# Kernel tuning notes

Measured on AMD Instinct MI355X. Metric: run time of the kernel, lower is better.

The kernel has to match this reference:

```python
import jax, jax.numpy as jnp
import numpy as np

B, N, RD = 32, 2000, 32
E, H, A = 128, 256, 8
NUM_ACTIONS = N
ACTION_NORM = float(NUM_ACTIONS)


def _mlp2(x, W1, b1, W2, b2):
    return jnp.maximum(x @ W1 + b1, 0.0) @ W2 + b2


def setup_inputs() -> dict:
    key = jax.random.key(0)
    ks = jax.random.split(key, 8)
    s = lambda fan_in: 1.0 / np.sqrt(fan_in)
    return {
        "state": jax.random.normal(ks[0], (B, N, RD), jnp.float32),
        "distance_matrix": jax.random.uniform(ks[1], (N, N), jnp.float32),
        "W_emb1": jax.random.normal(ks[2], (RD, H), jnp.float32) * s(RD),
        "b_emb1": jnp.zeros((H,), jnp.float32),
        "W_emb2": jax.random.normal(ks[3], (H, E), jnp.float32) * s(H),
        "b_emb2": jnp.zeros((E,), jnp.float32),
        "Wq1": jax.random.normal(ks[4], (E + A, H), jnp.float32) * s(E + A),
        "bq1": jnp.zeros((H,), jnp.float32),
        "Wq2": jax.random.normal(ks[5], (H, 1), jnp.float32) * s(H),
        "bq2": jnp.zeros((1,), jnp.float32),
        "fixed_actions": jax.random.randint(ks[6], (3, B), 0, NUM_ACTIONS, jnp.int32),
        "fixed_agent_ids": jnp.arange(3, dtype=jnp.int32),
    }


def reference(state, distance_matrix, W_emb1, b_emb1, W_emb2, b_emb2,
              Wq1, bq1, Wq2, bq2, fixed_actions, fixed_agent_ids):
    # normalized distance -> similarity, row-stochastic
    dm = distance_matrix / distance_matrix.max()
    sim = jnp.exp(-dm)  # scaling = 1 (use_nn_scaling=False)
    sim = sim / sim.sum(-1, keepdims=True)

    enc = _mlp2(state, W_emb1, b_emb1, W_emb2, b_emb2)      # [B,N,E]
    x = jnp.einsum('nm,bme->bne', sim, enc)                 # graph conv mix

    idx_f = jnp.arange(N, dtype=x.dtype)

    def qnet(actions):
        # actions: [B,A] broadcast over node axis -> concat -> MLP -> [B,N]
        act = jnp.broadcast_to(actions[:, None, :], (B, N, A))
        feat = jnp.concatenate([x, act], axis=-1)           # [B,N,E+A]
        return _mlp2(feat, Wq1, bq1, Wq2, bq2)[..., 0]      # [B,N]

    # init actions: -1 everywhere, fixed agents get given action / norm
    actions = jnp.full((B, A), -1.0, dtype=x.dtype)
    actions = actions.at[:, fixed_agent_ids].set(
        fixed_actions.T.astype(x.dtype) / ACTION_NORM)

    # sequential per-agent soft-argmax loop (second torch loop; the first
    # torch loop's q-values are fully overwritten here, so it is dead code)
    q_cols = []
    for agent_id in range(A):
        q = qnet(actions)                                   # [B,N]
        sam = jnp.clip(jax.nn.softmax(q, axis=-1) @ idx_f, 0.0, float(NUM_ACTIONS))
        actions = actions.at[:, agent_id].set(
            jax.lax.stop_gradient(sam / ACTION_NORM))
        q2 = qnet(actions)
        qv = jnp.take_along_axis(q2, sam.astype(jnp.int32)[:, None], axis=-1)[:, 0]
        q_cols.append(qv)

    q_values = jnp.stack(q_cols, axis=1)                    # [B,A]
    chosen = (actions * ACTION_NORM).astype(jnp.int32)      # [B,A]
    return q_values, chosen
```

## Files before the change

### kernel.cpp

```cpp
#include <hip/hip_runtime.h>
#include <cstddef>

#define NB 32
#define NN 2000
#define NRD 32
#define NE 128
#define NH 256
#define NA 8
#define KP8 2048
#define NGP 128
#define H1S 264
#define XTS 136
#define ACTION_NORM 2000.0f

typedef unsigned short u16;
typedef unsigned char u8;
typedef __bf16 b16x8 __attribute__((ext_vector_type(8)));
typedef float f32x4 __attribute__((ext_vector_type(4)));
typedef long lx2 __attribute__((ext_vector_type(2)));
typedef const __attribute__((address_space(1))) unsigned int* gptr_t;
typedef __attribute__((address_space(3))) unsigned int* lptr_t;

__device__ inline u16 f2bf(float x) {
    unsigned u = __float_as_uint(x);
    u += 0x7FFFu + ((u >> 16) & 1u);
    return (u16)(u >> 16);
}
__device__ inline float bf2f(u16 h) { return __uint_as_float((unsigned)h << 16); }
__device__ inline u8 f2fp8(float x) {
    return (u8)(__builtin_amdgcn_cvt_pk_fp8_f32(x, x, 0, false) & 0xFF);
}
__device__ inline u16 f2fp8x2(float a, float b) {
    return (u16)(__builtin_amdgcn_cvt_pk_fp8_f32(a, b, 0, false) & 0xFFFF);
}
__device__ inline float fp82f(u8 b) {
    return __builtin_amdgcn_cvt_pk_f32_fp8((unsigned)b, false)[0];
}
__device__ inline int kswz(int m) {
    return (m & ~63) + (((m >> 3) & 3) << 4) + (((m >> 5) & 1) << 3) + (m & 7);
}

#define PREP_STATE (64000 * 32)
#define PREP_W1T   (256 * 32)
#define PREP_W2T   (128 * 256)
#define PREP_WQ1T  (256 * 128)
#define PREP_PAD   (4096 * 48)
#define PREP_TOT   (PREP_STATE + PREP_W1T + PREP_W2T + PREP_WQ1T + PREP_PAD)
#define PREP_BLOCKS (PREP_TOT / 256)
#define MAX_BLOCKS 1024
__global__ __launch_bounds__(256) void k_front(
        const float* __restrict__ state, const float* __restrict__ W1,
        const float* __restrict__ W2, const float* __restrict__ Wq1,
        const float* __restrict__ dm, const int* __restrict__ fa,
        const int* __restrict__ fid,
        u16* __restrict__ state_b, u16* __restrict__ W1t,
        u16* __restrict__ W2t, u16* __restrict__ Wq1at,
        u8* __restrict__ encb, float* __restrict__ pmax,
        float* __restrict__ actions) {
    __shared__ float sh[256];
    const int blk = blockIdx.x, t = threadIdx.x;
    if (blk < PREP_BLOCKS) {
        int i = blk * 256 + t;
        if (i < PREP_STATE) { state_b[i] = f2bf(state[i]); return; }
        i -= PREP_STATE;
        if (i < PREP_W1T) { int h = i >> 5, k = i & 31; W1t[i] = f2bf(W1[k * NH + h]); return; }
        i -= PREP_W1T;
        if (i < PREP_W2T) { int e = i >> 8, h = i & 255; W2t[i] = f2bf(W2[h * NE + e]); return; }
        i -= PREP_W2T;
        if (i < PREP_WQ1T) { int hq = i >> 7, e = i & 127; Wq1at[i] = f2bf(Wq1[e * NH + hq]); return; }
        i -= PREP_WQ1T;
        if (i < PREP_PAD) { int eb = i / 48, mm = NN + (i % 48); encb[(size_t)eb * KP8 + kswz(mm)] = 0; }
        return;
    }
    if (blk < PREP_BLOCKS + MAX_BLOCKS) {
        const int bid = blk - PREP_BLOCKS;
        float m = 0.0f;
        for (size_t i = (size_t)bid * 256 + t; i < (size_t)NN * NN; i += (size_t)MAX_BLOCKS * 256)
            m = fmaxf(m, dm[i]);
        sh[t] = m; __syncthreads();
        for (int s = 128; s > 0; s >>= 1) {
            if (t < s) sh[t] = fmaxf(sh[t], sh[t + s]);
            __syncthreads();
        }
        if (t == 0) pmax[bid] = sh[0];
        return;
    }
    const int b = t >> 3, a = t & 7;
    float v = -1.0f;
    for (int j = 0; j < 3; ++j)
        if (fid[j] == a) v = (float)fa[j * NB + b] / ACTION_NORM;
    actions[t] = v;
}

__global__ __launch_bounds__(512) void k_sim_enc(
        const u16* __restrict__ state_b, const u16* __restrict__ W1t,
        const u16* __restrict__ W2t, u8* __restrict__ encb,
        const float* __restrict__ b1, const float* __restrict__ b2,
        const float* __restrict__ dm, const float* __restrict__ pmax,
        u8* __restrict__ simb, float* __restrict__ inv_rs) {
    __shared__ u16 stage[20 * 512];
    __shared__ u16 h1t[64 * H1S];
    const int blk = blockIdx.x, tid = threadIdx.x;

    if (blk >= 1000) {
        float* shf = (float*)stage;
        const int n = blk - 1000, t = tid;
        float m = fmaxf(pmax[t], pmax[t + 512]);
        shf[t] = m; __syncthreads();
        for (int s = 256; s > 0; s >>= 1) {
            if (t < s) shf[t] = fmaxf(shf[t], shf[t + s]);
            __syncthreads();
        }
        const float inv = 1.0f / shf[0];
        __syncthreads();
        float s = 0.0f;
        for (int mm = t * 2; mm < KP8; mm += 1024) {
            float e0 = 0.0f, e1 = 0.0f;
            if (mm < NN)     { e0 = expf(-dm[(size_t)n * NN + mm] * inv);     s += e0; }
            if (mm + 1 < NN) { e1 = expf(-dm[(size_t)n * NN + mm + 1] * inv); s += e1; }
            *(u16*)(simb + (size_t)n * KP8 + kswz(mm)) = f2fp8x2(e0, e1);
        }
        shf[t] = s; __syncthreads();
        for (int st = 256; st > 0; st >>= 1) {
            if (t < st) shf[t] += shf[t + st];
            __syncthreads();
        }
        if (t == 0) inv_rs[n] = 1.0f / shf[0];
        return;
    }

    const int w = tid >> 6, l = tid & 63;
    const int lm = l & 15, lq = l >> 4;
    const int gm = blk * 64;

    {
#pragma unroll
        for (int i = 0; i < 3; ++i) {
            const int idx = w * 3 + i;
            if (idx < 20) {
                const u16* gp;
                if (idx < 4) gp = state_b + (size_t)(gm + idx * 16 + lm) * NRD + lq * 8;
                else         gp = W1t + (size_t)((idx - 4) * 16 + lm) * NRD + lq * 8;
                __builtin_amdgcn_global_load_lds((gptr_t)gp, (lptr_t)(stage + idx * 512), 16, 0, 0);
            }
        }
        __syncthreads();
        b16x8 af[4], bf[2];
#pragma unroll
        for (int i = 0; i < 4; ++i) af[i] = *(const b16x8*)(stage + i * 512 + l * 8);
#pragma unroll
        for (int j = 0; j < 2; ++j) bf[j] = *(const b16x8*)(stage + (4 + w * 2 + j) * 512 + l * 8);
        f32x4 acc1[4][2] = {};
#pragma unroll
        for (int i = 0; i < 4; ++i)
#pragma unroll
            for (int j = 0; j < 2; ++j)
                acc1[i][j] = __builtin_amdgcn_mfma_f32_16x16x32_bf16(af[i], bf[j], acc1[i][j], 0, 0, 0);
#pragma unroll
        for (int i = 0; i < 4; ++i)
#pragma unroll
            for (int r = 0; r < 4; ++r) {
                const int row = i * 16 + lq * 4 + r;
#pragma unroll
                for (int j = 0; j < 2; ++j) {
                    const int col = w * 32 + j * 16 + lm;
                    h1t[row * H1S + col] = f2bf(fmaxf(acc1[i][j][r] + b1[col], 0.0f));
                }
            }
    }

    const int wr = w & 3, wc = w >> 2;
    f32x4 acc2[2][2] = {};
    for (int k0 = 0; k0 < NH; k0 += 32) {
        __syncthreads();
        {
            const u16* gp = W2t + (size_t)(w * 16 + lm) * NH + k0 + lq * 8;
            __builtin_amdgcn_global_load_lds((gptr_t)gp, (lptr_t)(stage + w * 512), 16, 0, 0);
        }
        __syncthreads();
        b16x8 af2[2], bf2[2];
#pragma unroll
        for (int i = 0; i < 2; ++i)
            af2[i] = *(const b16x8*)(stage + (wr * 2 + i) * 512 + l * 8);
#pragma unroll
        for (int j = 0; j < 2; ++j)
            bf2[j] = *(const b16x8*)(h1t + (wc * 32 + j * 16 + lm) * H1S + k0 + lq * 8);
#pragma unroll
        for (int i = 0; i < 2; ++i)
#pragma unroll
            for (int j = 0; j < 2; ++j)
                acc2[i][j] = __builtin_amdgcn_mfma_f32_16x16x32_bf16(af2[i], bf2[j], acc2[i][j], 0, 0, 0);
    }
#pragma unroll
    for (int i = 0; i < 2; ++i)
#pragma unroll
        for (int r = 0; r < 4; ++r) {
            const int e = wr * 32 + i * 16 + lq * 4 + r;
            const float bias = b2[e];
#pragma unroll
            for (int j = 0; j < 2; ++j) {
                const int rg = gm + wc * 32 + j * 16 + lm;
                const unsigned bb = (unsigned)rg / 2000u;
                const unsigned mm = (unsigned)rg - bb * 2000u;
                encb[((size_t)bb * 128 + e) * KP8 + kswz((int)mm)] = f2fp8(acc2[i][j][r] + bias);
            }
        }
}

__global__ __launch_bounds__(512) void k_conv_y0(
        const u8* __restrict__ simb, const u8* __restrict__ encb,
        const u16* __restrict__ Wq1at, const float* __restrict__ inv_rs,
        const float* __restrict__ bq1, u8* __restrict__ y0f8) {
    __shared__ u8 lds[16 * 1024];
    __shared__ u16 xt[128 * XTS];
    const int tid = threadIdx.x;
    const int w = tid >> 6, l = tid & 63;
    const int wr = w & 1, wc = w >> 1;
    const int bm = blockIdx.x * 128;
    const int bb = blockIdx.y;
    const int lm = l & 15, lq = l >> 4;
    const u8* Bt = encb + (size_t)bb * 128 * KP8;

    f32x4 acc[4][2] = {};

    for (int k0 = 0; k0 < KP8; k0 += 64) {
        __syncthreads();
#pragma unroll
        for (int i = 0; i < 2; ++i) {
            const int idx = w * 2 + i;
            const u8* gp;
            if (idx < 8) {
                int row = bm + idx * 16 + lm;
                row = row < NN ? row : NN - 1;
                gp = simb + (size_t)row * KP8 + k0 + lq * 16;
            } else {
                gp = Bt + (size_t)((idx - 8) * 16 + lm) * KP8 + k0 + lq * 16;
            }
            __builtin_amdgcn_global_load_lds((gptr_t)gp, (lptr_t)(lds + idx * 1024), 16, 0, 0);
        }
        __syncthreads();
        const int fo = l * 16;
        lx2 af[4], bf[2];
#pragma unroll
        for (int i = 0; i < 4; ++i)
            af[i] = *(const lx2*)(lds + (wr * 4 + i) * 1024 + fo);
#pragma unroll
        for (int j = 0; j < 2; ++j)
            bf[j] = *(const lx2*)(lds + (8 + wc * 2 + j) * 1024 + fo);
#pragma unroll
        for (int i = 0; i < 4; ++i)
#pragma unroll
            for (int j = 0; j < 2; ++j) {
                acc[i][j] = __builtin_amdgcn_mfma_f32_16x16x32_fp8_fp8(af[i][0], bf[j][0], acc[i][j], 0, 0, 0);
                acc[i][j] = __builtin_amdgcn_mfma_f32_16x16x32_fp8_fp8(af[i][1], bf[j][1], acc[i][j], 0, 0, 0);
            }
    }

    __syncthreads();
#pragma unroll
    for (int i = 0; i < 4; ++i) {
#pragma unroll
        for (int r = 0; r < 4; ++r) {
            const int row = wr * 64 + i * 16 + lq * 4 + r;
            const int gn = bm + row;
            const float rsv = inv_rs[gn < NN ? gn : NN - 1];
#pragma unroll
            for (int j = 0; j < 2; ++j) {
                const int col = wc * 32 + j * 16 + lm;
                xt[row * XTS + col] = f2bf(acc[i][j][r] * rsv);
            }
        }
    }
    __syncthreads();

    for (int half = 0; half < 2; ++half) {
        f32x4 acc2[4][2] = {};
#pragma unroll
        for (int ks = 0; ks < 4; ++ks) {
            b16x8 bfw[2];
#pragma unroll
            for (int j = 0; j < 2; ++j)
                bfw[j] = *(const b16x8*)(Wq1at + (size_t)(w * 32 + j * 16 + lm) * NE + ks * 32 + lq * 8);
#pragma unroll
            for (int i = 0; i < 4; ++i) {
                const b16x8 afx = *(const b16x8*)(xt + (half * 64 + i * 16 + lm) * XTS + ks * 32 + lq * 8);
#pragma unroll
                for (int j = 0; j < 2; ++j)
                    acc2[i][j] = __builtin_amdgcn_mfma_f32_16x16x32_bf16(afx, bfw[j], acc2[i][j], 0, 0, 0);
            }
        }
#pragma unroll
        for (int i = 0; i < 4; ++i) {
#pragma unroll
            for (int r = 0; r < 4; ++r) {
                const int n = bm + half * 64 + i * 16 + lq * 4 + r;
                if (n >= NN) continue;
#pragma unroll
                for (int j = 0; j < 2; ++j) {
                    const int h = w * 32 + j * 16 + lm;
                    y0f8[((size_t)n * NB + bb) * NH + h] = f2fp8(acc2[i][j][r] + bq1[h]);
                }
            }
        }
    }
}

__global__ __launch_bounds__(256) void k_agent(
        const u8* __restrict__ y0f8, const float* __restrict__ Wq1,
        const float* __restrict__ Wq2, const float* __restrict__ bq2,
        float* actions, const float2* __restrict__ pin, float2* __restrict__ pout,
        float* __restrict__ out, int ag) {
    __shared__ float sh[256];
    __shared__ float s_sam;
    const int t = threadIdx.x;
    const int lane = t & 63, wave = t >> 6;
    const int wg = blockIdx.x * 4 + wave;
    const int b = wg & 31, ng = wg >> 5;
    const int hl = lane & 15, qtr = lane >> 4;

    float act[NA];
#pragma unroll
    for (int a = 0; a < NA; ++a) act[a] = actions[b * NA + a];
    if (ag > 0) {
        const float2 p0 = pin[b * NGP + lane];
        const float2 p1 = pin[b * NGP + 64 + lane];
        float se0 = p0.x + p1.x, sn0 = p0.y + p1.y;
#pragma unroll
        for (int m = 32; m > 0; m >>= 1) {
            se0 += __shfl_xor(se0, m); sn0 += __shfl_xor(sn0, m);
        }
        const float sam = fminf(fmaxf(sn0 / se0, 0.0f), 2000.0f);
        act[ag - 1] = sam * (1.0f / ACTION_NORM);
    }
    float ap16[16] = {};
#pragma unroll
    for (int a = 0; a < NA; ++a) {
        const float av = act[a];
        const float4* wq = (const float4*)(Wq1 + (size_t)(NE + a) * NH + hl * 16);
#pragma unroll
        for (int jj = 0; jj < 4; ++jj) {
            const float4 w4 = wq[jj];
            ap16[jj * 4 + 0] = fmaf(av, w4.x, ap16[jj * 4 + 0]);
            ap16[jj * 4 + 1] = fmaf(av, w4.y, ap16[jj * 4 + 1]);
            ap16[jj * 4 + 2] = fmaf(av, w4.z, ap16[jj * 4 + 2]);
            ap16[jj * 4 + 3] = fmaf(av, w4.w, ap16[jj * 4 + 3]);
        }
    }
    float w2v[16];
    {
        const float4* w2p = (const float4*)(Wq2 + hl * 16);
#pragma unroll
        for (int jj = 0; jj < 4; ++jj) {
            const float4 w4 = w2p[jj];
            w2v[jj * 4 + 0] = w4.x; w2v[jj * 4 + 1] = w4.y;
            w2v[jj * 4 + 2] = w4.z; w2v[jj * 4 + 3] = w4.w;
        }
    }

    float se = 0.0f, sn = 0.0f;
#pragma unroll
    for (int k = 0; k < 4; ++k) {
        const int p = ng + k * NGP;
        if (p >= NN / 4) break;
        const int n = 4 * p + qtr;
        const uint4 yv = *(const uint4*)(y0f8 + (((size_t)n * NB + b) << 8) + hl * 16);
        const unsigned dw[4] = {yv.x, yv.y, yv.z, yv.w};
        float q = 0.0f;
#pragma unroll
        for (int d = 0; d < 4; ++d) {
            const auto lo = __builtin_amdgcn_cvt_pk_f32_fp8(dw[d], false);
            const auto hi = __builtin_amdgcn_cvt_pk_f32_fp8(dw[d], true);
            q += fmaxf(lo[0] + ap16[d * 4 + 0], 0.f) * w2v[d * 4 + 0];
            q += fmaxf(lo[1] + ap16[d * 4 + 1], 0.f) * w2v[d * 4 + 1];
            q += fmaxf(hi[0] + ap16[d * 4 + 2], 0.f) * w2v[d * 4 + 2];
            q += fmaxf(hi[1] + ap16[d * 4 + 3], 0.f) * w2v[d * 4 + 3];
        }
#pragma unroll
        for (int off = 1; off < 16; off <<= 1) q += __shfl_xor(q, off);
        const float e = expf(fminf(q, 60.0f));
        se += e; sn += e * (float)n;
    }
    se += __shfl_xor(se, 16); sn += __shfl_xor(sn, 16);
    se += __shfl_xor(se, 32); sn += __shfl_xor(sn, 32);
    if (lane == 0) pout[b * NGP + ng] = make_float2(se, sn);

    if (ag > 0 && blockIdx.x < NB) {
        const int bb = blockIdx.x;
        if (wave == 0) {
            const float2 p0 = pin[bb * NGP + lane];
            const float2 p1 = pin[bb * NGP + 64 + lane];
            float a1 = p0.x + p1.x, a2 = p0.y + p1.y;
#pragma unroll
            for (int m = 32; m > 0; m >>= 1) {
                a1 += __shfl_xor(a1, m); a2 += __shfl_xor(a2, m);
            }
            if (lane == 0) s_sam = fminf(fmaxf(a2 / a1, 0.0f), 2000.0f);
        }
        __syncthreads();
        const float sam = s_sam;
        const float samn = sam * (1.0f / ACTION_NORM);
        float apt = 0.0f;
#pragma unroll
        for (int a = 0; a < NA; ++a) {
            const float av = (a == ag - 1) ? samn : actions[bb * NA + a];
            apt = fmaf(av, Wq1[(size_t)(NE + a) * NH + t], apt);
        }
        int nsel = (int)sam; if (nsel > NN - 1) nsel = NN - 1;
        const float yv = fp82f(y0f8[((size_t)nsel * NB + bb) * NH + t]);
        sh[t] = fmaxf(yv + apt, 0.0f) * Wq2[t];
        __syncthreads();
        for (int s = 128; s > 0; s >>= 1) {
            if (t < s) sh[t] += sh[t + s];
            __syncthreads();
        }
        if (t == 0) {
            out[bb * NA + (ag - 1)] = sh[0] + bq2[0];
            actions[bb * NA + (ag - 1)] = samn;
        }
    }
}

__global__ __launch_bounds__(256) void k_fin(
        const u8* __restrict__ y0f8, const float* __restrict__ Wq1,
        const float* __restrict__ Wq2, const float* __restrict__ bq2,
        const float* __restrict__ actions, const float2* __restrict__ pin,
        float* __restrict__ out) {
    __shared__ float sh[256];
    __shared__ float s_sam;
    const int bb = blockIdx.x, t = threadIdx.x;
    const int lane = t & 63, wave = t >> 6;
    if (wave == 0) {
        const float2 p0 = pin[bb * NGP + lane];
        const float2 p1 = pin[bb * NGP + 64 + lane];
        float a1 = p0.x + p1.x, a2 = p0.y + p1.y;
#pragma unroll
        for (int m = 32; m > 0; m >>= 1) {
            a1 += __shfl_xor(a1, m); a2 += __shfl_xor(a2, m);
        }
        if (lane == 0) s_sam = fminf(fmaxf(a2 / a1, 0.0f), 2000.0f);
    }
    __syncthreads();
    const float sam = s_sam;
    const float samn = sam * (1.0f / ACTION_NORM);
    float apt = 0.0f;
#pragma unroll
    for (int a = 0; a < NA; ++a) {
        const float av = (a == NA - 1) ? samn : actions[bb * NA + a];
        apt = fmaf(av, Wq1[(size_t)(NE + a) * NH + t], apt);
    }
    int nsel = (int)sam; if (nsel > NN - 1) nsel = NN - 1;
    const float yv = fp82f(y0f8[((size_t)nsel * NB + bb) * NH + t]);
    sh[t] = fmaxf(yv + apt, 0.0f) * Wq2[t];
    __syncthreads();
    for (int s = 128; s > 0; s >>= 1) {
        if (t < s) sh[t] += sh[t + s];
        __syncthreads();
    }
    if (t == 0) out[bb * NA + (NA - 1)] = sh[0] + bq2[0];
    if (t < NA) {
        const float av = (t == NA - 1) ? samn : actions[bb * NA + t];
        out[NB * NA + bb * NA + t] = (float)(int)(av * ACTION_NORM);
    }
}

extern "C" void kernel_launch(void* const* d_in, const int* in_sizes, int n_in,
                              void* d_out, int out_size, void* d_ws, size_t ws_size,
                              hipStream_t stream) {
    const float* state = (const float*)d_in[0];
    const float* dm    = (const float*)d_in[1];
    const float* W1    = (const float*)d_in[2];
    const float* b1    = (const float*)d_in[3];
    const float* W2    = (const float*)d_in[4];
    const float* b2    = (const float*)d_in[5];
    const float* Wq1   = (const float*)d_in[6];
    const float* bq1   = (const float*)d_in[7];
    const float* Wq2   = (const float*)d_in[8];
    const float* bq2   = (const float*)d_in[9];
    const int* fa      = (const int*)d_in[10];
    const int* fid     = (const int*)d_in[11];
    float* out = (float*)d_out;

    char* p = (char*)d_ws;
    u8* simb       = (u8*)p;       p += (size_t)NN * KP8;
    u8* encb       = (u8*)p;       p += (size_t)4096 * KP8;
    float* inv_rs  = (float*)p;    p += 2048 * 4;
    float* pmax    = (float*)p;    p += 1024 * 4;
    float* actions = (float*)p;    p += 256 * 4;
    float2* part0  = (float2*)p;   p += (size_t)NB * NGP * 8;
    float2* part1  = (float2*)p;   p += (size_t)NB * NGP * 8;
    u16* state_b   = (u16*)p;      p += (size_t)2048000 * 2;
    u16* W1t       = (u16*)p;      p += 8192 * 2;
    u16* W2t       = (u16*)p;      p += 32768 * 2;
    u16* Wq1at     = (u16*)p;      p += 32768 * 2;
    u8* y0f8       = (u8*)p;       p += (size_t)16384000;

    k_front<<<PREP_BLOCKS + MAX_BLOCKS + 1, 256, 0, stream>>>(
        state, W1, W2, Wq1, dm, fa, fid,
        state_b, W1t, W2t, Wq1at, encb, pmax, actions);
    k_sim_enc<<<3000, 512, 0, stream>>>(state_b, W1t, W2t, encb, b1, b2,
                                        dm, pmax, simb, inv_rs);
    k_conv_y0<<<dim3(16, 32), 512, 0, stream>>>(simb, encb, Wq1at, inv_rs, bq1, y0f8);

    for (int ag = 0; ag < NA; ++ag) {
        const float2* pin  = (ag & 1) ? part0 : part1;
        float2*       pout = (ag & 1) ? part1 : part0;
        k_agent<<<1024, 256, 0, stream>>>(y0f8, Wq1, Wq2, bq2, actions,
                                          pin, pout, out, ag);
    }
    k_fin<<<NB, 256, 0, stream>>>(y0f8, Wq1, Wq2, bq2, actions, part1, out);
}
```

Before: 273.0 us.

## Fuse first agent's softmax partials into conv kernel and use fp8 for Q-layer GEMM

Computes the initial action projection in the front kernel and folds the first agent's q-value/softmax partial-sum computation into the conv_y0 epilogue. This removes one k_agent launch and its full pass over y0. The second-layer GEMM in conv_y0 now uses fp8 MFMA with fp8 weights and fp8 x staging instead of bf16, which halves operand bytes but adds quantization error to the q-values. The conv_y0 kernel gains extra reductions and block syncs in exchange.

```diff
diff --git a/kernel.cpp b/kernel.cpp
--- a/kernel.cpp
+++ b/kernel.cpp
@@ -10,14 +10,13 @@
 #define KP8 2048
 #define NGP 128
 #define H1S 264
-#define XTS 136
+#define XT8S 136
 #define ACTION_NORM 2000.0f
 
 typedef unsigned short u16;
 typedef unsigned char u8;
 typedef __bf16 b16x8 __attribute__((ext_vector_type(8)));
 typedef float f32x4 __attribute__((ext_vector_type(4)));
-typedef long lx2 __attribute__((ext_vector_type(2)));
 typedef const __attribute__((address_space(1))) unsigned int* gptr_t;
 typedef __attribute__((address_space(3))) unsigned int* lptr_t;
 
@@ -54,9 +53,10 @@
         const float* __restrict__ dm, const int* __restrict__ fa,
         const int* __restrict__ fid,
         u16* __restrict__ state_b, u16* __restrict__ W1t,
-        u16* __restrict__ W2t, u16* __restrict__ Wq1at,
+        u16* __restrict__ W2t, u8* __restrict__ Wq1f8,
         u8* __restrict__ encb, float* __restrict__ pmax,
-        float* __restrict__ actions) {
+        float* __restrict__ actions, float* __restrict__ ap0,
+        float2* __restrict__ part0) {
     __shared__ float sh[256];
     const int blk = blockIdx.x, t = threadIdx.x;
     if (blk < PREP_BLOCKS) {
@@ -67,7 +67,7 @@
         i -= PREP_W1T;
         if (i < PREP_W2T) { int e = i >> 8, h = i & 255; W2t[i] = f2bf(W2[h * NE + e]); return; }
         i -= PREP_W2T;
-        if (i < PREP_WQ1T) { int hq = i >> 7, e = i & 127; Wq1at[i] = f2bf(Wq1[e * NH + hq]); return; }
+        if (i < PREP_WQ1T) { int hq = i >> 7, e = i & 127; Wq1f8[i] = f2fp8(Wq1[e * NH + hq]); return; }
         i -= PREP_WQ1T;
         if (i < PREP_PAD) { int eb = i / 48, mm = NN + (i % 48); encb[(size_t)eb * KP8 + kswz(mm)] = 0; }
         return;
@@ -90,6 +90,18 @@
     for (int j = 0; j < 3; ++j)
         if (fid[j] == a) v = (float)fa[j * NB + b] / ACTION_NORM;
     actions[t] = v;
+    sh[t] = v;
+    __syncthreads();
+    float wq[NA];
+#pragma unroll
+    for (int aa = 0; aa < NA; ++aa) wq[aa] = Wq1[(size_t)(NE + aa) * NH + t];
+    for (int bb = 0; bb < NB; ++bb) {
+        float s = 0.0f;
+#pragma unroll
+        for (int aa = 0; aa < NA; ++aa) s = fmaf(sh[bb * NA + aa], wq[aa], s);
+        ap0[bb * NH + t] = s;
+    }
+    for (int i = t; i < NB * NGP; i += 256) part0[i] = make_float2(0.0f, 0.0f);
 }
 
 __global__ __launch_bounds__(512) void k_sim_enc(
@@ -209,10 +221,13 @@
 
 __global__ __launch_bounds__(512) void k_conv_y0(
         const u8* __restrict__ simb, const u8* __restrict__ encb,
-        const u16* __restrict__ Wq1at, const float* __restrict__ inv_rs,
-        const float* __restrict__ bq1, u8* __restrict__ y0f8) {
+        const u8* __restrict__ Wq1f8, const float* __restrict__ inv_rs,
+        const float* __restrict__ bq1, const float* __restrict__ ap0,
+        const float* __restrict__ Wq2, u8* __restrict__ y0f8,
+        float2* __restrict__ part0) {
     __shared__ u8 lds[16 * 1024];
-    __shared__ u16 xt[128 * XTS];
+    __shared__ u8 xt8[128 * XT8S];
+    __shared__ float qsum[64 * 8];
     const int tid = threadIdx.x;
     const int w = tid >> 6, l = tid & 63;
     const int wr = w & 1, wc = w >> 1;
@@ -240,6 +255,7 @@
         }
         __syncthreads();
         const int fo = l * 16;
+        typedef long lx2 __attribute__((ext_vector_type(2)));
         lx2 af[4], bf[2];
 #pragma unroll
         for (int i = 0; i < 4; ++i)
@@ -267,42 +283,74 @@
 #pragma unroll
             for (int j = 0; j < 2; ++j) {
                 const int col = wc * 32 + j * 16 + lm;
-                xt[row * XTS + col] = f2bf(acc[i][j][r] * rsv);
+                xt8[row * XT8S + col] = f2fp8(acc[i][j][r] * rsv);
             }
         }
     }
     __syncthreads();
+
+    const int h0 = w * 32;
+    float bq1v[2], apv[2], w2vv[2];
+#pragma unroll
+    for (int j = 0; j < 2; ++j) {
+        const int h = h0 + j * 16 + lm;
+        bq1v[j] = bq1[h];
+        apv[j] = ap0[bb * NH + h];
+        w2vv[j] = Wq2[h];
+    }
+    float se_tot = 0.0f, sn_tot = 0.0f;
 
     for (int half = 0; half < 2; ++half) {
         f32x4 acc2[4][2] = {};
 #pragma unroll
         for (int ks = 0; ks < 4; ++ks) {
-            b16x8 bfw[2];
+            long bfw[2];
 #pragma unroll
             for (int j = 0; j < 2; ++j)
-                bfw[j] = *(const b16x8*)(Wq1at + (size_t)(w * 32 + j * 16 + lm) * NE + ks * 32 + lq * 8);
+                bfw[j] = *(const long*)(Wq1f8 + (size_t)(h0 + j * 16 + lm) * NE + ks * 32 + lq * 8);
 #pragma unroll
             for (int i = 0; i < 4; ++i) {
-                const b16x8 afx = *(const b16x8*)(xt + (half * 64 + i * 16 + lm) * XTS + ks * 32 + lq * 8);
+                const long afx = *(const long*)(xt8 + (half * 64 + i * 16 + lm) * XT8S + ks * 32 + lq * 8);
 #pragma unroll
                 for (int j = 0; j < 2; ++j)
-                    acc2[i][j] = __builtin_amdgcn_mfma_f32_16x16x32_bf16(afx, bfw[j], acc2[i][j], 0, 0, 0);
+                    acc2[i][j] = __builtin_amdgcn_mfma_f32_16x16x32_fp8_fp8(afx, bfw[j], acc2[i][j], 0, 0, 0);
             }
         }
 #pragma unroll
         for (int i = 0; i < 4; ++i) {
 #pragma unroll
             for (int r = 0; r < 4; ++r) {
-                const int n = bm + half * 64 + i * 16 + lq * 4 + r;
-                if (n >= NN) continue;
+                const int rl = i * 16 + lq * 4 + r;
+                const int n = bm + half * 64 + rl;
+                float q = 0.0f;
 #pragma unroll
                 for (int j = 0; j < 2; ++j) {
-                    const int h = w * 32 + j * 16 + lm;
-                    y0f8[((size_t)n * NB + bb) * NH + h] = f2fp8(acc2[i][j][r] + bq1[h]);
+                    const float v = acc2[i][j][r] + bq1v[j];
+                    if (n < NN) y0f8[((size_t)n * NB + bb) * NH + h0 + j * 16 + lm] = f2fp8(v);
+                    q += fmaxf(v + apv[j], 0.0f) * w2vv[j];
                 }
-            }
-        }
-    }
+#pragma unroll
+                for (int off = 1; off < 16; off <<= 1) q += __shfl_xor(q, off);
+                if (lm == 0) qsum[rl * 8 + w] = q;
+            }
+        }
+        __syncthreads();
+        if (tid < 64) {
+            const int n = bm + half * 64 + tid;
+            float q = 0.0f;
+#pragma unroll
+            for (int wv = 0; wv < 8; ++wv) q += qsum[tid * 8 + wv];
+            float e = (n < NN) ? expf(fminf(q, 60.0f)) : 0.0f;
+            float sne = e * (float)n;
+#pragma unroll
+            for (int off = 32; off > 0; off >>= 1) {
+                e += __shfl_xor(e, off); sne += __shfl_xor(sne, off);
+            }
+            if (tid == 0) { se_tot += e; sn_tot += sne; }
+        }
+        __syncthreads();
+    }
+    if (tid == 0) part0[bb * NGP + blockIdx.x] = make_float2(se_tot, sn_tot);
 }
 
 __global__ __launch_bounds__(256) void k_agent(
@@ -321,7 +369,7 @@
     float act[NA];
 #pragma unroll
     for (int a = 0; a < NA; ++a) act[a] = actions[b * NA + a];
-    if (ag > 0) {
+    {
         const float2 p0 = pin[b * NGP + lane];
         const float2 p1 = pin[b * NGP + 64 + lane];
         float se0 = p0.x + p1.x, sn0 = p0.y + p1.y;
@@ -384,7 +432,7 @@
     se += __shfl_xor(se, 32); sn += __shfl_xor(sn, 32);
     if (lane == 0) pout[b * NGP + ng] = make_float2(se, sn);
 
-    if (ag > 0 && blockIdx.x < NB) {
+    if (blockIdx.x < NB) {
         const int bb = blockIdx.x;
         if (wave == 0) {
             const float2 p0 = pin[bb * NGP + lane];
@@ -486,22 +534,23 @@
     float* inv_rs  = (float*)p;    p += 2048 * 4;
     float* pmax    = (float*)p;    p += 1024 * 4;
     float* actions = (float*)p;    p += 256 * 4;
+    float* ap0     = (float*)p;    p += 8192 * 4;
     float2* part0  = (float2*)p;   p += (size_t)NB * NGP * 8;
     float2* part1  = (float2*)p;   p += (size_t)NB * NGP * 8;
     u16* state_b   = (u16*)p;      p += (size_t)2048000 * 2;
     u16* W1t       = (u16*)p;      p += 8192 * 2;
     u16* W2t       = (u16*)p;      p += 32768 * 2;
-    u16* Wq1at     = (u16*)p;      p += 32768 * 2;
+    u8* Wq1f8      = (u8*)p;       p += 32768;
     u8* y0f8       = (u8*)p;       p += (size_t)16384000;
 
     k_front<<<PREP_BLOCKS + MAX_BLOCKS + 1, 256, 0, stream>>>(
         state, W1, W2, Wq1, dm, fa, fid,
-        state_b, W1t, W2t, Wq1at, encb, pmax, actions);
+        state_b, W1t, W2t, Wq1f8, encb, pmax, actions, ap0, part0);
     k_sim_enc<<<3000, 512, 0, stream>>>(state_b, W1t, W2t, encb, b1, b2,
                                         dm, pmax, simb, inv_rs);
-    k_conv_y0<<<dim3(16, 32), 512, 0, stream>>>(simb, encb, Wq1at, inv_rs, bq1, y0f8);
-
-    for (int ag = 0; ag < NA; ++ag) {
+    k_conv_y0<<<dim3(16, 32), 512, 0, stream>>>(simb, encb, Wq1f8, inv_rs, bq1,
+                                                ap0, Wq2, y0f8, part0);
+    for (int ag = 1; ag < NA; ++ag) {
         const float2* pin  = (ag & 1) ? part0 : part1;
         float2*       pout = (ag & 1) ? part1 : part0;
         k_agent<<<1024, 256, 0, stream>>>(y0f8, Wq1, Wq2, bq2, actions,
```

Result: faster. 260.2 us (-4.7%).
